# Performance work log

Measured on AMD Instinct MI355X. Metric: run time of the kernel, lower is better.

The kernel has to match this reference:

```python
import jax, jax.numpy as jnp
import numpy as np

B, RX, RXA, TX, TXA = 32, 1, 16, 1, 4
NT, L = 2048, 16
T = NT + L - 1  # 2063 output time samples


def _toeplitz_indices():
    # g[i, j] = i - j if in [0, NT), else NT (points at the zero pad)
    idx = np.arange(T)[:, None] - np.arange(L)[None, :]
    return jnp.asarray(np.where((idx >= 0) & (idx < NT), idx, NT), jnp.int32)


def setup_inputs() -> dict:
    key = jax.random.key(0)
    k1, k2 = jax.random.split(key)
    x = jax.random.normal(k1, (B, TX, TXA, NT), jnp.float32)
    h_time = jax.random.normal(k2, (B, RX, RXA, TX, TXA, T, L), jnp.float32)
    return {"x": x, "h_time": h_time, "g": _toeplitz_indices()}


def reference(x, h_time, g):
    # pad one zero sample at the end of the time axis
    xp = jnp.pad(x, ((0, 0), (0, 0), (0, 0), (0, 1)))  # [B,TX,TXA,NT+1]
    # Toeplitz gather (im2col of sliding windows): [B,TX,TXA,T,L]
    xg = xp[..., g]
    # multiply by channel taps and reduce over taps (l), tx antennas (a), tx (t)
    # h_time: [b,r,c,t,a,m,l]; xg: [b,t,a,m,l] -> y: [b,r,c,m]
    y = jnp.einsum('brctaml,btaml->brcm', h_time, xg)
    return y
```

## Files before the change

### kernel.cpp

```cpp
#include <hip/hip_runtime.h>


#define NTT 2048
#define LL  16
#define TT  2063
#define NC  16
#define NA  4
#define BM  256
#define MT  ((TT + BM - 1) / BM)

typedef float f32x4 __attribute__((ext_vector_type(4)));

__global__ __launch_bounds__(BM) void atc_kernel(
    const float* __restrict__ x,
    const float* __restrict__ h,
    float* __restrict__ y)
{
    __shared__ float xs[NA][BM + LL];

    const int bid = blockIdx.x;
    const int mt  = bid % MT;
    const int c   = (bid / MT) % NC;
    const int b   = bid / (MT * NC);
    const int m0  = mt * BM;
    const int tid = threadIdx.x;

    const int WIN = BM + LL - 1;
    for (int i = tid; i < NA * WIN; i += BM) {
        const int a = i / WIN;
        const int j = i - a * WIN;
        const int tg = m0 - (LL - 1) + j;
        float v = 0.0f;
        if (tg >= 0 && tg < NTT) v = x[(b * NA + a) * NTT + tg];
        xs[a][j] = v;
    }
    __syncthreads();

    const int m = m0 + tid;
    if (m < TT) {
        const f32x4* hp = reinterpret_cast<const f32x4*>(
            h + ((size_t)(b * NC + c) * NA * TT + m) * LL);
        const size_t astride = (size_t)TT * LL / 4;
        f32x4 hr[NA][4];
        #pragma unroll
        for (int a = 0; a < NA; ++a) {
            #pragma unroll
            for (int k = 0; k < 4; ++k) {
                hr[a][k] = __builtin_nontemporal_load(&hp[(size_t)a * astride + k]);
            }
        }

        float acc0 = 0.f, acc1 = 0.f, acc2 = 0.f, acc3 = 0.f;
        #pragma unroll
        for (int a = 0; a < NA; ++a) {
            const float* xw = &xs[a][tid];
            acc0 += hr[a][0].x * xw[15] + hr[a][0].y * xw[14] + hr[a][0].z * xw[13] + hr[a][0].w * xw[12];
            acc1 += hr[a][1].x * xw[11] + hr[a][1].y * xw[10] + hr[a][1].z * xw[ 9] + hr[a][1].w * xw[ 8];
            acc2 += hr[a][2].x * xw[ 7] + hr[a][2].y * xw[ 6] + hr[a][2].z * xw[ 5] + hr[a][2].w * xw[ 4];
            acc3 += hr[a][3].x * xw[ 3] + hr[a][3].y * xw[ 2] + hr[a][3].z * xw[ 1] + hr[a][3].w * xw[ 0];
        }
        y[(size_t)(b * NC + c) * TT + m] = (acc0 + acc1) + (acc2 + acc3);
    }
}

extern "C" void kernel_launch(void* const* d_in, const int* in_sizes, int n_in,
                              void* d_out, int out_size, void* d_ws, size_t ws_size,
                              hipStream_t stream) {
    const float* x = (const float*)d_in[0];
    const float* h = (const float*)d_in[1];
    float* y = (float*)d_out;

    const int nblocks = 32 * NC * MT;
    atc_kernel<<<nblocks, BM, 0, stream>>>(x, h, y);
}
```

Measured before the change: 376.1 us.

## Split each output's taps across four lanes for coalesced h loads

```diff
diff --git a/kernel.cpp b/kernel.cpp
--- a/kernel.cpp
+++ b/kernel.cpp
@@ -6,60 +6,58 @@
 #define TT  2063
 #define NC  16
 #define NA  4
-#define BM  256
-#define MT  ((TT + BM - 1) / BM)
+#define BMQ 64
+#define MT  ((TT + BMQ - 1) / BMQ)
 
 typedef float f32x4 __attribute__((ext_vector_type(4)));
 
-__global__ __launch_bounds__(BM) void atc_kernel(
+__global__ __launch_bounds__(256) void atc_kernel(
     const float* __restrict__ x,
     const float* __restrict__ h,
     float* __restrict__ y)
 {
-    __shared__ float xs[NA][BM + LL];
+    __shared__ float xs[NA][BMQ + LL];
 
     const int bid = blockIdx.x;
     const int mt  = bid % MT;
     const int c   = (bid / MT) % NC;
     const int b   = bid / (MT * NC);
-    const int m0  = mt * BM;
+    const int m0  = mt * BMQ;
     const int tid = threadIdx.x;
+    const int q   = tid & 3;
+    const int ml  = tid >> 2;
 
-    const int WIN = BM + LL - 1;
-    for (int i = tid; i < NA * WIN; i += BM) {
+    const int WIN = BMQ + LL - 1;
+    for (int i = tid; i < NA * WIN; i += 256) {
         const int a = i / WIN;
         const int j = i - a * WIN;
         const int tg = m0 - (LL - 1) + j;
-        float v = 0.0f;
-        if (tg >= 0 && tg < NTT) v = x[(b * NA + a) * NTT + tg];
-        xs[a][j] = v;
+        xs[a][j] = (tg >= 0 && tg < NTT) ? x[(b * NA + a) * NTT + tg] : 0.0f;
     }
     __syncthreads();
 
-    const int m = m0 + tid;
+    const int m = m0 + ml;
+    float acc = 0.0f;
     if (m < TT) {
         const f32x4* hp = reinterpret_cast<const f32x4*>(
-            h + ((size_t)(b * NC + c) * NA * TT + m) * LL);
+            h + ((size_t)(b * NC + c) * NA * TT + m) * LL) + q;
         const size_t astride = (size_t)TT * LL / 4;
-        f32x4 hr[NA][4];
+        f32x4 hv[NA];
+        #pragma unroll
+        for (int a = 0; a < NA; ++a) hv[a] = hp[(size_t)a * astride];
+
         #pragma unroll
         for (int a = 0; a < NA; ++a) {
-            #pragma unroll
-            for (int k = 0; k < 4; ++k) {
-                hr[a][k] = __builtin_nontemporal_load(&hp[(size_t)a * astride + k]);
-            }
+            const float* xw = &xs[a][ml + (LL - 1) - 4 * q];
+            acc += hv[a].x * xw[0] + hv[a].y * xw[-1]
+                 + hv[a].z * xw[-2] + hv[a].w * xw[-3];
         }
+    }
 
-        float acc0 = 0.f, acc1 = 0.f, acc2 = 0.f, acc3 = 0.f;
-        #pragma unroll
-        for (int a = 0; a < NA; ++a) {
-            const float* xw = &xs[a][tid];
-            acc0 += hr[a][0].x * xw[15] + hr[a][0].y * xw[14] + hr[a][0].z * xw[13] + hr[a][0].w * xw[12];
-            acc1 += hr[a][1].x * xw[11] + hr[a][1].y * xw[10] + hr[a][1].z * xw[ 9] + hr[a][1].w * xw[ 8];
-            acc2 += hr[a][2].x * xw[ 7] + hr[a][2].y * xw[ 6] + hr[a][2].z * xw[ 5] + hr[a][2].w * xw[ 4];
-            acc3 += hr[a][3].x * xw[ 3] + hr[a][3].y * xw[ 2] + hr[a][3].z * xw[ 1] + hr[a][3].w * xw[ 0];
-        }
-        y[(size_t)(b * NC + c) * TT + m] = (acc0 + acc1) + (acc2 + acc3);
+    acc += __shfl_xor(acc, 1);
+    acc += __shfl_xor(acc, 2);
+    if (q == 0 && m < TT) {
+        y[(size_t)(b * NC + c) * TT + m] = acc;
     }
 }
 
@@ -71,5 +69,5 @@
     float* y = (float*)d_out;
 
     const int nblocks = 32 * NC * MT;
-    atc_kernel<<<nblocks, BM, 0, stream>>>(x, h, y);
+    atc_kernel<<<nblocks, 256, 0, stream>>>(x, h, y);
 }
```

After: 359.1 us. 1.05x faster.
